# Performance work log

Measured on AMD Instinct MI355X. Metric: run time of the kernel, lower is better.

## Reference

```python
import jax, jax.numpy as jnp
import numpy as np

N_NODES = 50000
N_EDGES = 800000
IN_CH = 256
OUT_CH = 64
HEADS = 4


def setup_inputs() -> dict:
    key = jax.random.key(0)
    k1, k2, k3, k4, k5 = jax.random.split(key, 5)
    x = jax.random.normal(k1, (N_NODES, IN_CH), dtype=jnp.float32)
    edge_index = jax.random.randint(k2, (2, N_EDGES), 0, N_NODES, dtype=jnp.int64)
    # xavier-ish scaled params
    weight = jax.random.normal(k3, (HEADS, IN_CH, OUT_CH), dtype=jnp.float32) * (2.0 / (IN_CH + OUT_CH)) ** 0.5
    att_src = jax.random.normal(k4, (1, HEADS, OUT_CH), dtype=jnp.float32) * 0.1
    att_dst = jax.random.normal(k5, (1, HEADS, OUT_CH), dtype=jnp.float32) * 0.1
    bias = jnp.zeros((HEADS * OUT_CH,), dtype=jnp.float32)
    return {"x": x, "edge_index": edge_index, "weight": weight,
            "att_src": att_src, "att_dst": att_dst, "bias": bias}


def reference(x, edge_index, weight, att_src, att_dst, bias):
    # GATConv forward (eval mode: dropout is identity), vectorized over heads.
    num_nodes = x.shape[0]
    row, col = edge_index[0], edge_index[1]
    # per-head projection: [N, H, C]
    x_h = jnp.einsum('nf,hfc->nhc', x, weight)
    alpha_src = jnp.sum(x_h * att_src[0], axis=-1)   # [N, H]
    alpha_dst = jnp.sum(x_h * att_dst[0], axis=-1)   # [N, H]
    alpha = alpha_src[row] + alpha_dst[col]          # [E, H]
    alpha = jax.nn.leaky_relu(alpha, negative_slope=0.2)
    # segment softmax over edges grouped by destination row (numerically stable)
    alpha_max = jax.ops.segment_max(alpha, row, num_segments=num_nodes)  # [N, H]
    alpha = jnp.exp(alpha - alpha_max[row])
    alpha_sum = jax.ops.segment_sum(alpha, row, num_segments=num_nodes)  # [N, H]
    alpha = alpha / jnp.clip(alpha_sum[row], 1e-16)
    # message passing: scatter-add alpha-weighted source features
    messages = alpha[:, :, None] * x_h[col]                              # [E, H, C]
    out = jax.ops.segment_sum(messages, row, num_segments=num_nodes)    # [N, H, C]
    out = out.reshape(num_nodes, -1) + bias                              # concat heads
    return out
```

## Files before the change

kernel.cpp:

```cpp
#include <hip/hip_runtime.h>
#include <hip/hip_fp16.h>
#include <math.h>

#define N_IN_CH 256
#define N_OUT   256
#define HEADS   4
#define OUT_CH  64
#define BM      64
#define SCAN_BLOCK 1024

typedef __attribute__((ext_vector_type(8))) short bf16x8;
typedef __attribute__((ext_vector_type(4))) float f32x4;

__device__ __forceinline__ float lrelu(float a) {
  return a >= 0.f ? a : 0.2f * a;
}

__device__ __forceinline__ ushort f2bf(float f) {
  uint u = __float_as_uint(f);
  uint r = (u + 0x7FFFu + ((u >> 16) & 1u)) >> 16;
  return (ushort)r;
}

__device__ __forceinline__ ushort f2h(float f) {
  return __half_as_ushort(__float2half(f));
}
__device__ __forceinline__ float h2f(ushort u) {
  return __half2float(__ushort_as_half(u));
}

__device__ __forceinline__ int wave_scan_partials(const int* __restrict__ partials,
                                                  int nparts, int lane) {
  int pv = (lane < nparts) ? partials[lane] : 0;
  int incl = pv;
#pragma unroll
  for (int d = 1; d < 64; d <<= 1) {
    int t = __shfl_up(incl, d, 64);
    if (lane >= d) incl += t;
  }
  return incl - pv;
}

__global__ void convert_w(const float* __restrict__ w, ushort* __restrict__ bt,
                          int* __restrict__ counts, int nnodes) {
  const int idx = blockIdx.x * 256 + threadIdx.x;
  if (idx < nnodes) counts[idx] = 0;
  const int n = idx >> 8, k = idx & 255;
  const int h = n >> 6, c = n & 63;
  bt[idx] = f2bf(w[h * (N_IN_CH * OUT_CH) + k * OUT_CH + c]);
}

__global__ __launch_bounds__(256) void proj_count(
    const float* __restrict__ x, const ushort* __restrict__ bt,
    const float* __restrict__ att_src, const float* __restrict__ att_dst,
    ushort* __restrict__ xh, float* __restrict__ asrc, float* __restrict__ adst,
    int nnodes, int nblocksA,
    const int* __restrict__ row, int* __restrict__ counts,
    int* __restrict__ rank, int nedges) {
  __shared__ ushort at[BM * N_IN_CH];
  const int tid = threadIdx.x;

  if (blockIdx.x >= nblocksA) {
    const int e = (blockIdx.x - nblocksA) * 256 + tid;
    if (e < nedges) rank[e] = atomicAdd(&counts[row[e]], 1);
    return;
  }

  const int wave = tid >> 6;
  const int lane = tid & 63;
  const int n0 = blockIdx.x * BM;

  {
    const int rsub = tid >> 6;
    const int cf = (tid & 63) * 4;
    const int cb = cf * 2;
#pragma unroll
    for (int it = 0; it < 16; ++it) {
      const int row_ = it * 4 + rsub;
      const int grow = n0 + row_;
      float4 xv = make_float4(0.f, 0.f, 0.f, 0.f);
      if (grow < nnodes) xv = *(const float4*)&x[(size_t)grow * N_IN_CH + cf];
      ushort4 b;
      b.x = f2bf(xv.x); b.y = f2bf(xv.y); b.z = f2bf(xv.z); b.w = f2bf(xv.w);
      const int cbs = cb ^ ((row_ & 7) << 4);
      *(ushort4*)((char*)at + row_ * 512 + cbs) = b;
    }
  }
  __syncthreads();

  f32x4 acc[4][4];
#pragma unroll
  for (int mt = 0; mt < 4; ++mt)
#pragma unroll
    for (int nt = 0; nt < 4; ++nt) acc[mt][nt] = (f32x4){0.f, 0.f, 0.f, 0.f};

  const int lmod = lane & 15;
  const int ldiv = lane >> 4;

  for (int ks = 0; ks < 8; ++ks) {
    bf16x8 a[4], b[4];
#pragma unroll
    for (int mt = 0; mt < 4; ++mt) {
      const int row_ = mt * 16 + lmod;
      const int kb = ks * 64 + ldiv * 16;
      const int cbs = kb ^ ((row_ & 7) << 4);
      a[mt] = *(const bf16x8*)((const char*)at + row_ * 512 + cbs);
    }
#pragma unroll
    for (int nt = 0; nt < 4; ++nt) {
      const int n = wave * 64 + nt * 16 + lmod;
      b[nt] = *(const bf16x8*)&bt[(size_t)n * N_IN_CH + ks * 32 + ldiv * 8];
    }
#pragma unroll
    for (int mt = 0; mt < 4; ++mt)
#pragma unroll
      for (int nt = 0; nt < 4; ++nt)
        acc[mt][nt] = __builtin_amdgcn_mfma_f32_16x16x32_bf16(
            a[mt], b[nt], acc[mt][nt], 0, 0, 0);
  }

  float atts[4], attd[4];
#pragma unroll
  for (int nt = 0; nt < 4; ++nt) {
    const int gcol = wave * 64 + nt * 16 + lmod;
    atts[nt] = att_src[gcol];
    attd[nt] = att_dst[gcol];
  }

#pragma unroll
  for (int mt = 0; mt < 4; ++mt) {
#pragma unroll
    for (int reg = 0; reg < 4; ++reg) {
      const int grow = n0 + mt * 16 + ldiv * 4 + reg;
      const bool ok = grow < nnodes;
      float vs = 0.f, vd = 0.f;
#pragma unroll
      for (int nt = 0; nt < 4; ++nt) {
        const float v = acc[mt][nt][reg];
        if (ok) xh[(size_t)grow * N_OUT + wave * 64 + nt * 16 + lmod] = f2h(v);
        vs = fmaf(v, atts[nt], vs);
        vd = fmaf(v, attd[nt], vd);
      }
#pragma unroll
      for (int d = 1; d < 16; d <<= 1) {
        vs += __shfl_xor(vs, d, 64);
        vd += __shfl_xor(vd, d, 64);
      }
      if (lmod == 0 && ok) {
        asrc[grow * HEADS + wave] = vs;
        adst[grow * HEADS + wave] = vd;
      }
    }
  }
}

__global__ __launch_bounds__(SCAN_BLOCK) void scan1_kernel(
    const int* __restrict__ counts, int* __restrict__ offsets,
    int* __restrict__ partials, int n) {
  __shared__ int wsum[16];
  const int tid = threadIdx.x;
  const int lane = tid & 63;
  const int wid = tid >> 6;
  const int i = blockIdx.x * SCAN_BLOCK + tid;
  int v = (i < n) ? counts[i] : 0;
  int incl = v;
#pragma unroll
  for (int d = 1; d < 64; d <<= 1) {
    int t = __shfl_up(incl, d, 64);
    if (lane >= d) incl += t;
  }
  if (lane == 63) wsum[wid] = incl;
  __syncthreads();
  if (wid == 0) {
    int wv = (lane < 16) ? wsum[lane] : 0;
#pragma unroll
    for (int d = 1; d < 16; d <<= 1) {
      int t = __shfl_up(wv, d, 64);
      if (lane >= d) wv += t;
    }
    if (lane < 16) wsum[lane] = wv;
  }
  __syncthreads();
  const int wexcl = (wid == 0) ? 0 : wsum[wid - 1];
  if (i <= n) offsets[i] = wexcl + incl - v;
  if (tid == SCAN_BLOCK - 1) partials[blockIdx.x] = wsum[15];
}

__global__ void scatter_kernel(const int* __restrict__ row, const int* __restrict__ col,
                               const int* __restrict__ rank,
                               const int* __restrict__ offsets,
                               const int* __restrict__ partials, int nparts,
                               const float* __restrict__ asrc,
                               const float* __restrict__ adst,
                               uint4* __restrict__ erec, int nedges) {
  const int lane = threadIdx.x & 63;
  const int excl = wave_scan_partials(partials, nparts, lane);
  int e = blockIdx.x * blockDim.x + threadIdx.x;
  if (e < nedges) {
    const int r = row[e];
    const int c = col[e];
    const int pos = offsets[r] + __shfl(excl, r >> 10, 64) + rank[e];
    const float4 s = *(const float4*)&asrc[r * 4];
    const float4 d = *(const float4*)&adst[c * 4];
    uint4 rec;
    rec.x = (uint)c;
    rec.y = (uint)f2h(__expf(lrelu(s.x + d.x))) |
            ((uint)f2h(__expf(lrelu(s.y + d.y))) << 16);
    rec.z = (uint)f2h(__expf(lrelu(s.z + d.z))) |
            ((uint)f2h(__expf(lrelu(s.w + d.w))) << 16);
    rec.w = 0u;
    erec[pos] = rec;
  }
}

__global__ __launch_bounds__(256) void gather_kernel(
    const int* __restrict__ offsets,
    const int* __restrict__ partials, int nparts,
    const uint4* __restrict__ erec,
    const ushort* __restrict__ xh, const float* __restrict__ bias,
    float* __restrict__ out, int nnodes) {
  __shared__ float pbuf[4][64 * 4];
  const int wv = threadIdx.x >> 6;
  const int lane = threadIdx.x & 63;
  const int n = blockIdx.x * 4 + wv;
  if (n >= nnodes) return;
  const int excl = wave_scan_partials(partials, nparts, lane);
  const int off = offsets[n] + __shfl(excl, n >> 10, 64);
  const int end = offsets[n + 1] + __shfl(excl, (n + 1) >> 10, 64);
  const int deg = end - off;
  const int half = lane >> 5;
  const int ch8 = (lane & 31) * 8;
  const int hh = (lane & 31) >> 3;

  float4 s4 = make_float4(0.f, 0.f, 0.f, 0.f);
  float a0 = 0.f, a1 = 0.f, a2 = 0.f, a3 = 0.f;
  float a4 = 0.f, a5 = 0.f, a6 = 0.f, a7 = 0.f;

  for (int b = 0; b < deg; b += 64) {
    const int cnt = min(64, deg - b);
    int cl_l = 0;
    float4 p = make_float4(0.f, 0.f, 0.f, 0.f);
    if (lane < cnt) {
      const uint4 rec = erec[off + b + lane];
      cl_l = (int)rec.x;
      p.x = h2f((ushort)(rec.y & 0xFFFFu));
      p.y = h2f((ushort)(rec.y >> 16));
      p.z = h2f((ushort)(rec.z & 0xFFFFu));
      p.w = h2f((ushort)(rec.z >> 16));
      s4.x += p.x; s4.y += p.y; s4.z += p.z; s4.w += p.w;
    }
    *(float4*)&pbuf[wv][lane * 4] = p;

    for (int j = 0; j < cnt; j += 16) {
      int cq[8];
#pragma unroll
      for (int q = 0; q < 8; ++q) cq[q] = __shfl(cl_l, j + 2 * q + half, 64);
      uint4 xq[8];
#pragma unroll
      for (int q = 0; q < 8; ++q)
        xq[q] = *(const uint4*)&xh[(size_t)cq[q] * N_OUT + ch8];

      float wq[8];
#pragma unroll
      for (int q = 0; q < 8; ++q) wq[q] = pbuf[wv][(j + 2 * q + half) * 4 + hh];

#pragma unroll
      for (int q = 0; q < 8; ++q) {
        a0 = fmaf(wq[q], h2f((ushort)(xq[q].x & 0xFFFFu)), a0);
        a1 = fmaf(wq[q], h2f((ushort)(xq[q].x >> 16)), a1);
        a2 = fmaf(wq[q], h2f((ushort)(xq[q].y & 0xFFFFu)), a2);
        a3 = fmaf(wq[q], h2f((ushort)(xq[q].y >> 16)), a3);
        a4 = fmaf(wq[q], h2f((ushort)(xq[q].z & 0xFFFFu)), a4);
        a5 = fmaf(wq[q], h2f((ushort)(xq[q].z >> 16)), a5);
        a6 = fmaf(wq[q], h2f((ushort)(xq[q].w & 0xFFFFu)), a6);
        a7 = fmaf(wq[q], h2f((ushort)(xq[q].w >> 16)), a7);
      }
    }
  }

  a0 += __shfl_xor(a0, 32, 64);
  a1 += __shfl_xor(a1, 32, 64);
  a2 += __shfl_xor(a2, 32, 64);
  a3 += __shfl_xor(a3, 32, 64);
  a4 += __shfl_xor(a4, 32, 64);
  a5 += __shfl_xor(a5, 32, 64);
  a6 += __shfl_xor(a6, 32, 64);
  a7 += __shfl_xor(a7, 32, 64);

#pragma unroll
  for (int d = 1; d < 64; d <<= 1) {
    s4.x += __shfl_xor(s4.x, d, 64);
    s4.y += __shfl_xor(s4.y, d, 64);
    s4.z += __shfl_xor(s4.z, d, 64);
    s4.w += __shfl_xor(s4.w, d, 64);
  }
  const float sh = (hh == 0) ? s4.x : (hh == 1) ? s4.y : (hh == 2) ? s4.z : s4.w;
  const float invh = 1.f / fmaxf(sh, 1e-16f);

  const int wch = ch8 + half * 4;
  const float4 b4 = *(const float4*)&bias[wch];
  float4 o;
  o.x = fmaf(half ? a4 : a0, invh, b4.x);
  o.y = fmaf(half ? a5 : a1, invh, b4.y);
  o.z = fmaf(half ? a6 : a2, invh, b4.z);
  o.w = fmaf(half ? a7 : a3, invh, b4.w);
  *(float4*)&out[(size_t)n * N_OUT + wch] = o;
}

extern "C" void kernel_launch(void* const* d_in, const int* in_sizes, int n_in,
                              void* d_out, int out_size, void* d_ws, size_t ws_size,
                              hipStream_t stream) {
  const float* x        = (const float*)d_in[0];
  const int*   edge_idx = (const int*)d_in[1];
  const float* weight   = (const float*)d_in[2];
  const float* att_src  = (const float*)d_in[3];
  const float* att_dst  = (const float*)d_in[4];
  const float* bias     = (const float*)d_in[5];
  float* out = (float*)d_out;

  const int nnodes = in_sizes[0] / N_IN_CH;
  const int nedges = in_sizes[1] / 2;
  const int* row = edge_idx;
  const int* col = edge_idx + nedges;

  char* wsb = (char*)d_ws;
  size_t woff = 0;
  auto alloc = [&](size_t bytes) -> char* {
    char* p = wsb + woff;
    woff += (bytes + 255) & ~(size_t)255;
    return p;
  };
  ushort* xh    = (ushort*)alloc((size_t)nnodes * N_OUT * sizeof(ushort));
  ushort* bt    = (ushort*)alloc((size_t)N_OUT * N_IN_CH * sizeof(ushort));
  float* asrc   = (float*)alloc((size_t)nnodes * HEADS * sizeof(float));
  float* adst   = (float*)alloc((size_t)nnodes * HEADS * sizeof(float));
  int* counts   = (int*)alloc((size_t)nnodes * sizeof(int));
  int* offsets  = (int*)alloc((size_t)(nnodes + 1) * sizeof(int));
  int* partials = (int*)alloc(256 * sizeof(int));
  int* rank     = (int*)alloc((size_t)nedges * sizeof(int));
  uint4* erec   = (uint4*)alloc((size_t)nedges * sizeof(uint4));

  convert_w<<<256, 256, 0, stream>>>(weight, bt, counts, nnodes);

  const int eblocks = (nedges + 255) / 256;
  const int nblocksA = (nnodes + BM - 1) / BM;
  proj_count<<<nblocksA + eblocks, 256, 0, stream>>>(
      x, bt, att_src, att_dst, xh, asrc, adst, nnodes, nblocksA,
      row, counts, rank, nedges);

  const int nscan = (nnodes + 1 + SCAN_BLOCK - 1) / SCAN_BLOCK;
  scan1_kernel<<<nscan, SCAN_BLOCK, 0, stream>>>(counts, offsets, partials, nnodes);

  scatter_kernel<<<eblocks, 256, 0, stream>>>(row, col, rank, offsets,
                                              partials, nscan,
                                              asrc, adst, erec, nedges);

  gather_kernel<<<(nnodes + 3) / 4, 256, 0, stream>>>(offsets, partials, nscan,
                                                      erec, xh, bias, out, nnodes);
}
```

Baseline: 160.7 us.

## Move edge counting to its own kernel and fuse scan into projection launch

Edge-degree counting with atomics now runs as a separate kernel before the projection. The per-block prefix scan of counts moves into extra blocks of the projection launch, using 256 threads that each handle 4 elements. This removes the standalone scan launch and overlaps the scan with the GEMM instead of overlapping counting with it. The trade is that the atomic counting no longer overlaps the projection and now runs serially in front of it.

After: 165.9 us. 3.2% more time.

```diff
diff --git a/kernel.cpp b/kernel.cpp
--- a/kernel.cpp
+++ b/kernel.cpp
@@ -7,7 +7,7 @@
 #define HEADS   4
 #define OUT_CH  64
 #define BM      64
-#define SCAN_BLOCK 1024
+#define SCAN_ELEMS 1024
 
 typedef __attribute__((ext_vector_type(8))) short bf16x8;
 typedef __attribute__((ext_vector_type(4))) float f32x4;
@@ -50,19 +50,52 @@
   bt[idx] = f2bf(w[h * (N_IN_CH * OUT_CH) + k * OUT_CH + c]);
 }
 
-__global__ __launch_bounds__(256) void proj_count(
+__global__ void count_kernel(const int* __restrict__ row, int* __restrict__ counts,
+                             int* __restrict__ rank, int nedges) {
+  int e = blockIdx.x * blockDim.x + threadIdx.x;
+  if (e < nedges) rank[e] = atomicAdd(&counts[row[e]], 1);
+}
+
+__global__ __launch_bounds__(256) void proj_scan(
     const float* __restrict__ x, const ushort* __restrict__ bt,
     const float* __restrict__ att_src, const float* __restrict__ att_dst,
     ushort* __restrict__ xh, float* __restrict__ asrc, float* __restrict__ adst,
     int nnodes, int nblocksA,
-    const int* __restrict__ row, int* __restrict__ counts,
-    int* __restrict__ rank, int nedges) {
+    const int* __restrict__ counts, int* __restrict__ offsets,
+    int* __restrict__ partials) {
   __shared__ ushort at[BM * N_IN_CH];
   const int tid = threadIdx.x;
 
   if (blockIdx.x >= nblocksA) {
-    const int e = (blockIdx.x - nblocksA) * 256 + tid;
-    if (e < nedges) rank[e] = atomicAdd(&counts[row[e]], 1);
+    __shared__ int wsum[4];
+    const int sb = blockIdx.x - nblocksA;
+    const int base = sb * SCAN_ELEMS + tid * 4;
+    const int n = nnodes;
+    int v0 = (base + 0 < n) ? counts[base + 0] : 0;
+    int v1 = (base + 1 < n) ? counts[base + 1] : 0;
+    int v2 = (base + 2 < n) ? counts[base + 2] : 0;
+    int v3 = (base + 3 < n) ? counts[base + 3] : 0;
+    const int tsum = v0 + v1 + v2 + v3;
+    const int lane = tid & 63;
+    const int wid = tid >> 6;
+    int incl = tsum;
+#pragma unroll
+    for (int d = 1; d < 64; d <<= 1) {
+      int t = __shfl_up(incl, d, 64);
+      if (lane >= d) incl += t;
+    }
+    if (lane == 63) wsum[wid] = incl;
+    __syncthreads();
+    int wexcl = incl - tsum;
+    int bexcl = 0;
+#pragma unroll
+    for (int wq = 0; wq < 4; ++wq) bexcl += (wq < wid) ? wsum[wq] : 0;
+    const int te = bexcl + wexcl;
+    if (base + 0 <= n) offsets[base + 0] = te;
+    if (base + 1 <= n) offsets[base + 1] = te + v0;
+    if (base + 2 <= n) offsets[base + 2] = te + v0 + v1;
+    if (base + 3 <= n) offsets[base + 3] = te + v0 + v1 + v2;
+    if (tid == 0) partials[sb] = wsum[0] + wsum[1] + wsum[2] + wsum[3];
     return;
   }
 
@@ -152,38 +185,6 @@
       }
     }
   }
-}
-
-__global__ __launch_bounds__(SCAN_BLOCK) void scan1_kernel(
-    const int* __restrict__ counts, int* __restrict__ offsets,
-    int* __restrict__ partials, int n) {
-  __shared__ int wsum[16];
-  const int tid = threadIdx.x;
-  const int lane = tid & 63;
-  const int wid = tid >> 6;
-  const int i = blockIdx.x * SCAN_BLOCK + tid;
-  int v = (i < n) ? counts[i] : 0;
-  int incl = v;
-#pragma unroll
-  for (int d = 1; d < 64; d <<= 1) {
-    int t = __shfl_up(incl, d, 64);
-    if (lane >= d) incl += t;
-  }
-  if (lane == 63) wsum[wid] = incl;
-  __syncthreads();
-  if (wid == 0) {
-    int wv = (lane < 16) ? wsum[lane] : 0;
-#pragma unroll
-    for (int d = 1; d < 16; d <<= 1) {
-      int t = __shfl_up(wv, d, 64);
-      if (lane >= d) wv += t;
-    }
-    if (lane < 16) wsum[lane] = wv;
-  }
-  __syncthreads();
-  const int wexcl = (wid == 0) ? 0 : wsum[wid - 1];
-  if (i <= n) offsets[i] = wexcl + incl - v;
-  if (tid == SCAN_BLOCK - 1) partials[blockIdx.x] = wsum[15];
 }
 
 __global__ void scatter_kernel(const int* __restrict__ row, const int* __restrict__ col,
@@ -343,13 +344,13 @@
   convert_w<<<256, 256, 0, stream>>>(weight, bt, counts, nnodes);
 
   const int eblocks = (nedges + 255) / 256;
+  count_kernel<<<eblocks, 256, 0, stream>>>(row, counts, rank, nedges);
+
   const int nblocksA = (nnodes + BM - 1) / BM;
-  proj_count<<<nblocksA + eblocks, 256, 0, stream>>>(
+  const int nscan = (nnodes + 1 + SCAN_ELEMS - 1) / SCAN_ELEMS;
+  proj_scan<<<nblocksA + nscan, 256, 0, stream>>>(
       x, bt, att_src, att_dst, xh, asrc, adst, nnodes, nblocksA,
-      row, counts, rank, nedges);
-
-  const int nscan = (nnodes + 1 + SCAN_BLOCK - 1) / SCAN_BLOCK;
-  scan1_kernel<<<nscan, SCAN_BLOCK, 0, stream>>>(counts, offsets, partials, nnodes);
+      counts, offsets, partials);
 
   scatter_kernel<<<eblocks, 256, 0, stream>>>(row, col, rank, offsets,
                                               partials, nscan,
```
